# Performance work log

Measured on AMD Instinct MI355X. Metric: run time of the kernel, lower is better.

The kernel has to match this reference:

```python
import jax, jax.numpy as jnp
import numpy as np

S, B, DIN = 3, 4096, 1024
H1, H2, H3, D = 512, 384, 256, 128
K, C = 512, 3            # codebook size, n_codebooks
TEMP = 0.1               # contrastive temperature
EPS = 1e-12


def setup_inputs() -> dict:
    key = jax.random.key(0)
    ks = jax.random.split(key, 16)
    g = lambda k, shp, s=0.05: (jax.random.normal(k, shp, dtype=jnp.float32) * s)
    return {
        'x': jax.random.normal(ks[0], (S, B, DIN), dtype=jnp.float32),
        'enc_w1': g(ks[1], (S, DIN, H1)), 'enc_b1': g(ks[2], (S, H1)),
        'enc_w2': g(ks[3], (S, H1, H2)), 'enc_b2': g(ks[4], (S, H2)),
        'enc_w3': g(ks[5], (S, H2, H3)), 'enc_b3': g(ks[6], (S, H3)),
        'enc_w4': g(ks[7], (S, H3, D)),  'enc_b4': g(ks[8], (S, D)),
        'q_w1': g(ks[9], (D, D)), 'q_b1': g(ks[10], (D,)),
        'q_w2': g(ks[11], (D,)),
        'codebooks': jax.random.normal(ks[12], (C, K, D), dtype=jnp.float32),
    }


def _normalize(v):
    return v / jnp.maximum(jnp.linalg.norm(v, axis=-1, keepdims=True), EPS)


def _forward(x, enc_w1, enc_b1, enc_w2, enc_b2, enc_w3, enc_b3,
             enc_w4, enc_b4, q_w1, q_b1, q_w2, codebooks):
    sg = jax.lax.stop_gradient
    # per-source MLP encoders (stacked over source axis s)
    h = jax.nn.relu(jnp.einsum('sbi,sio->sbo', x, enc_w1) + enc_b1[:, None, :])
    h = jax.nn.relu(jnp.einsum('sbi,sio->sbo', h, enc_w2) + enc_b2[:, None, :])
    h = jax.nn.relu(jnp.einsum('sbi,sio->sbo', h, enc_w3) + enc_b3[:, None, :])
    emb = jnp.einsum('sbi,sio->sbo', h, enc_w4) + enc_b4[:, None, :]  # [S,B,D]

    # attention fusion: Linear->Tanh->Linear(1) per source, softmax over sources
    score = jnp.einsum('sbd,d->sb', jnp.tanh(jnp.einsum('sbd,de->sbe', emb, q_w1) + q_b1), q_w2)
    weight = jax.nn.softmax(score.T, axis=-1)                # [B,S]
    fused = jnp.einsum('bs,sbd->bd', weight, emb)            # [B,D]

    # residual VQ over C codebooks (straight-through, MSE losses)
    res = fused
    q_sum = jnp.zeros_like(fused)
    commit_loss = jnp.float32(0.0)
    for k in range(C):
        e = codebooks[k]                                     # [K,D]
        d2 = (jnp.sum(res * res, axis=1, keepdims=True)
              - 2.0 * res @ e.T + jnp.sum(e * e, axis=1))    # [B,K]
        ids = jnp.argmin(d2, axis=1)
        q = e[ids]                                           # [B,D]
        commit_loss = commit_loss + jnp.mean((sg(q) - res) ** 2)
        q_st = res + sg(q - res)                             # straight-through
        q_sum = q_sum + q_st
        res = res - q_st

    # codebook regularizer: mean pairwise cosine gram of normalized codebooks
    cbn = _normalize(codebooks)
    codebook_loss = jnp.mean(jnp.einsum('mkd,mjd->mkj', cbn, cbn))

    # contrastive losses (projection = identity)
    z1 = _normalize(q_sum)                                   # [B,D]
    contrast = []
    for s in range(S):
        z2 = _normalize(emb[s])
        refl = jnp.exp((z1 @ z1.T) / TEMP)                   # [B,B]
        between = jnp.exp((z1 @ z2.T) / TEMP)
        pos = jnp.diagonal(between)
        denom = refl.sum(1) + between.sum(1) - jnp.diagonal(refl)
        contrast.append(jnp.mean(-jnp.log(pos / denom)))

    return jnp.stack([1.0 * codebook_loss, 0.0 * commit_loss] + contrast)


def reference(x, enc_w1, enc_b1, enc_w2, enc_b2, enc_w3, enc_b3,
              enc_w4, enc_b4, q_w1, q_b1, q_w2, codebooks):
    return _forward(x, enc_w1, enc_b1, enc_w2, enc_b2, enc_w3, enc_b3,
                    enc_w4, enc_b4, q_w1, q_b1, q_w2, codebooks)
```

## Files before the change

kernel.cpp:

```cpp
#include <hip/hip_runtime.h>
#include <hip/hip_bf16.h>

#define S_   3
#define B_   4096
#define DIN_ 1024
#define H1_  512
#define H2_  384
#define H3_  256
#define D_   128
#define K_   512
#define C_   3
#define INV_T 10.0f
#define EPS_  1e-12f
#define EXP10 22026.465794806718f

typedef float f32x4 __attribute__((ext_vector_type(4)));
typedef short bf16x8 __attribute__((ext_vector_type(8)));

__device__ __forceinline__ unsigned short f2bf(float f) {
  unsigned int u = __float_as_uint(f);
  u = (u + 0x7FFF + ((u >> 16) & 1)) >> 16;
  return (unsigned short)u;
}

__device__ __forceinline__ void gl2lds16(const unsigned short* g, unsigned short* l) {
  __builtin_amdgcn_global_load_lds(
      (const __attribute__((address_space(1))) void*)g,
      (__attribute__((address_space(3))) void*)l, 16, 0, 0);
}

__device__ __forceinline__ float waveReduceSum(float v) {
#pragma unroll
  for (int off = 32; off > 0; off >>= 1) v += __shfl_down(v, off, 64);
  return v;
}

__device__ __forceinline__ float waveXorSum(float v) {
#pragma unroll
  for (int off = 32; off > 0; off >>= 1) v += __shfl_xor(v, off, 64);
  return v;
}

__global__ __launch_bounds__(256) void prep_kernel(
    const float* __restrict__ x, unsigned short* __restrict__ xb,
    const float* __restrict__ w1, unsigned short* __restrict__ wt1,
    const float* __restrict__ w2, unsigned short* __restrict__ wt2,
    const float* __restrict__ w3, unsigned short* __restrict__ wt3,
    const float* __restrict__ w4, unsigned short* __restrict__ w4tb,
    const float* __restrict__ cb, float* __restrict__ cbn2,
    float* __restrict__ cbsumP, unsigned short* __restrict__ cbb,
    const float* __restrict__ qw1, unsigned short* __restrict__ qw1tb) {
  __shared__ float tt[32][33];
  __shared__ float invn[64];
  const int t = threadIdx.x;
  int blk = blockIdx.x;
  const int NCVT = (S_ * B_ * DIN_) / 1024;
  if (blk < NCVT) {
    int i = (blk * 256 + t) * 4;
    float4 v = *(const float4*)(x + i);
    xb[i + 0] = f2bf(v.x); xb[i + 1] = f2bf(v.y);
    xb[i + 2] = f2bf(v.z); xb[i + 3] = f2bf(v.w);
    return;
  }
  blk -= NCVT;
  const int NT = 1536 + 576 + 288 + 96;
  if (blk >= NT) {
    int cblk = blk - NT;
    if (cblk < 24) {
      const int m = cblk >> 3;
      const int k0 = (cblk & 7) * 64;
      const int w = t >> 6, lane = t & 63;
      for (int r = w * 16; r < w * 16 + 16; r++) {
        int k = k0 + r;
        float2 v = *(const float2*)(cb + ((size_t)m * K_ + k) * D_ + lane * 2);
        unsigned short* crow = cbb + ((size_t)m * K_ + k) * D_;
        crow[lane * 2 + 0] = f2bf(v.x);
        crow[lane * 2 + 1] = f2bf(v.y);
        float n2 = waveXorSum(v.x * v.x + v.y * v.y);
        if (lane == 0) {
          cbn2[m * K_ + k] = n2;
          invn[r] = 1.0f / fmaxf(sqrtf(n2), EPS_);
        }
      }
      __syncthreads();
      if (t < D_) {
        float acc = 0.0f;
        for (int r = 0; r < 64; r++)
          acc += cb[((size_t)m * K_ + k0 + r) * D_ + t] * invn[r];
        cbsumP[(size_t)cblk * D_ + t] = acc;
      }
      return;
    }
    cblk -= 24;
    const int kx = cblk & 3, ny = cblk >> 2;
    const int k0 = kx * 32, n0 = ny * 32;
    const int tx = t & 31, ty = t >> 5;
#pragma unroll
    for (int i = 0; i < 4; i++)
      tt[ty + 8 * i][tx] = qw1[(size_t)(k0 + ty + 8 * i) * D_ + n0 + tx];
    __syncthreads();
#pragma unroll
    for (int i = 0; i < 4; i++)
      qw1tb[(size_t)(n0 + ty + 8 * i) * D_ + k0 + tx] = f2bf(tt[tx][ty + 8 * i]);
    return;
  }
  const float* W; unsigned short* Wt; int K, N; int plain = 0;
  if (blk < 1536) { W = w1; Wt = wt1; K = DIN_; N = H1_; }
  else {
    blk -= 1536;
    if (blk < 576) { W = w2; Wt = wt2; K = H1_; N = H2_; }
    else {
      blk -= 576;
      if (blk < 288) { W = w3; Wt = wt3; K = H2_; N = H3_; }
      else { blk -= 288; W = w4; Wt = w4tb; K = H3_; N = D_; plain = 1; }
    }
  }
  const int kx_n = K / 32, ny_n = N / 32;
  const int kx = blk % kx_n;
  const int ny = (blk / kx_n) % ny_n;
  const int s  = blk / (kx_n * ny_n);
  const int k0 = kx * 32, n0 = ny * 32;
  const int tx = t & 31, ty = t >> 5;
  const float* Ws = W + (size_t)s * K * N;
  const int nb = N >> 7, kb = K >> 6;
#pragma unroll
  for (int i = 0; i < 4; i++)
    tt[ty + 8 * i][tx] = Ws[(size_t)(k0 + ty + 8 * i) * N + n0 + tx];
  __syncthreads();
  const int k = k0 + tx;
  if (plain) {
#pragma unroll
    for (int i = 0; i < 4; i++) {
      int n = n0 + ty + 8 * i;
      Wt[((size_t)(s * D_ + n)) * H3_ + k] = f2bf(tt[tx][ty + 8 * i]);
    }
  } else {
    const int kt = k >> 6, ksl = (k >> 5) & 1;
#pragma unroll
    for (int i = 0; i < 4; i++) {
      int n = n0 + ty + 8 * i;
      size_t dst = ((size_t)(s * nb + (n >> 7)) * kb + kt) * 8192 +
                   (size_t)ksl * 4096 + (size_t)(n & 127) * 32 + (k & 31);
      Wt[dst] = f2bf(tt[tx][ty + 8 * i]);
    }
  }
}

__global__ __launch_bounds__(256) void gemm_lds_kernel(
    const unsigned short* __restrict__ A, const unsigned short* __restrict__ Wsw,
    const float* __restrict__ bias, void* __restrict__ Y,
    int K, int N, int relu, int out_f32) {
  const int t = threadIdx.x;
  const int lane = t & 63;
  const int w = t >> 6;
  const int ln = lane & 15, q = lane >> 4;
  const int wm = w >> 1, wn = w & 1;
  const int n0 = blockIdx.x * 128;
  const int mblk = blockIdx.y;
  const int s = mblk >> 6;
  const int m0 = mblk * 64;
  const int nb = N >> 7, kb = K >> 6;

  const unsigned short* Ag = A + (size_t)m0 * K;
  const unsigned short* Bt = Wsw + ((size_t)(s * nb + blockIdx.x) * kb) * 8192;
  const float* bs = bias + (size_t)s * N;

  __shared__ unsigned short Asm[2 * 64 * 32];
  __shared__ unsigned short Bsm[2 * 8192];

  const int arow0 = t >> 3, ak8 = t & 7;
  const int aL0 = (ak8 >> 2) * 2048 + arow0 * 32 + (ak8 & 3) * 8;
  const size_t gA0 = (size_t)arow0 * K + ak8 * 8;

  bf16x8 ra0 = *(const bf16x8*)(Ag + gA0);
  bf16x8 ra1 = *(const bf16x8*)(Ag + gA0 + (size_t)32 * K);
#pragma unroll
  for (int p = 0; p < 4; p++)
    gl2lds16(Bt + (size_t)(p * 256 + t) * 8, &Bsm[(size_t)(p * 256 + t) * 8]);

  f32x4 acc[2][4];
#pragma unroll
  for (int i = 0; i < 2; i++)
#pragma unroll
    for (int j = 0; j < 4; j++) acc[i][j] = (f32x4){0.f, 0.f, 0.f, 0.f};

  for (int kt = 0; kt < kb; kt++) {
    *(bf16x8*)&Asm[aL0] = ra0;
    *(bf16x8*)&Asm[aL0 + 1024] = ra1;
    __syncthreads();
    const unsigned short* Bcur = &Bsm[(kt & 1) * 8192];
    if (kt + 1 < kb) {
      const unsigned short* Bn = Bt + (size_t)(kt + 1) * 8192;
      unsigned short* Bd = &Bsm[((kt + 1) & 1) * 8192];
#pragma unroll
      for (int p = 0; p < 4; p++)
        gl2lds16(Bn + (size_t)(p * 256 + t) * 8, Bd + (size_t)(p * 256 + t) * 8);
      const size_t g = gA0 + (size_t)(kt + 1) * 64;
      ra0 = *(const bf16x8*)(Ag + g);
      ra1 = *(const bf16x8*)(Ag + g + (size_t)32 * K);
    }
    bf16x8 af[2][2], bf[4][2];
#pragma unroll
    for (int ti = 0; ti < 2; ti++)
#pragma unroll
      for (int ksl = 0; ksl < 2; ksl++)
        af[ti][ksl] = *(const bf16x8*)&Asm[ksl * 2048 + (wm * 32 + ti * 16 + ln) * 32 + q * 8];
#pragma unroll
    for (int tj = 0; tj < 4; tj++)
#pragma unroll
      for (int ksl = 0; ksl < 2; ksl++)
        bf[tj][ksl] = *(const bf16x8*)&Bcur[ksl * 4096 + (wn * 64 + tj * 16 + ln) * 32 + q * 8];
#pragma unroll
    for (int ksl = 0; ksl < 2; ksl++)
#pragma unroll
      for (int ti = 0; ti < 2; ti++)
#pragma unroll
        for (int tj = 0; tj < 4; tj++)
          acc[ti][tj] = __builtin_amdgcn_mfma_f32_16x16x32_bf16(af[ti][ksl], bf[tj][ksl], acc[ti][tj], 0, 0, 0);
    __syncthreads();
  }

#pragma unroll
  for (int ti = 0; ti < 2; ti++)
#pragma unroll
    for (int tj = 0; tj < 4; tj++) {
      const int cc = n0 + wn * 64 + tj * 16 + ln;
      const float bv = bs[cc];
#pragma unroll
      for (int reg = 0; reg < 4; reg++) {
        const int r = m0 + wm * 32 + ti * 16 + q * 4 + reg;
        float v = acc[ti][tj][reg] + bv;
        if (relu) v = fmaxf(v, 0.0f);
        if (out_f32) ((float*)Y)[(size_t)r * N + cc] = v;
        else ((unsigned short*)Y)[(size_t)r * N + cc] = f2bf(v);
      }
    }
}

__global__ __launch_bounds__(512) void l4vq_kernel(
    const unsigned short* __restrict__ h3b, const unsigned short* __restrict__ w4tb,
    const float* __restrict__ b4, const unsigned short* __restrict__ qw1tb,
    const float* __restrict__ qb1, const float* __restrict__ qw2,
    const float* __restrict__ cb, const unsigned short* __restrict__ cbb,
    const float* __restrict__ cbn2,
    unsigned short* __restrict__ zb, float* __restrict__ pos) {
  const int b0 = blockIdx.x * 16;
  const int t = threadIdx.x;
  const int w = t >> 6, lane = t & 63;
  const int ln = lane & 15, q = lane >> 4;

  __shared__ unsigned short h3s[48][264];
  __shared__ float e[48][D_];
  __shared__ unsigned short ebb[48][136];
  __shared__ float qf[16][D_];
  __shared__ float resv[16][D_];
  __shared__ unsigned short resb[16][136];
  __shared__ float red2[8][48];
  __shared__ float sc[48];
  __shared__ float candd[8][16];
  __shared__ int candk[8][16];
  __shared__ int bestk[16];

  bf16x8 bq[4];
  {
    const unsigned short* qp = qw1tb + (size_t)(w * 16 + ln) * D_;
#pragma unroll
    for (int ks = 0; ks < 4; ks++)
      bq[ks] = *(const bf16x8*)(qp + ks * 32 + q * 8);
  }

#pragma unroll
  for (int p = 0; p < 3; p++) {
    int f = p * 512 + t;
    int r = f >> 5, kf = f & 31;
    int s = r >> 4, bi = r & 15;
    *(bf16x8*)&h3s[r][kf * 8] =
        *(const bf16x8*)(h3b + ((size_t)(s * B_ + b0 + bi)) * H3_ + kf * 8);
  }
  __syncthreads();

  {
    const int col = w * 16 + ln;
#pragma unroll
    for (int s = 0; s < 3; s++) {
      f32x4 oacc = (f32x4){0.f, 0.f, 0.f, 0.f};
      const unsigned short* wp = w4tb + ((size_t)(s * D_ + col)) * H3_;
#pragma unroll
      for (int ks = 0; ks < 8; ks++) {
        bf16x8 bfrag = *(const bf16x8*)(wp + ks * 32 + q * 8);
        bf16x8 afrag = *(const bf16x8*)&h3s[s * 16 + ln][ks * 32 + q * 8];
        oacc = __builtin_amdgcn_mfma_f32_16x16x32_bf16(afrag, bfrag, oacc, 0, 0, 0);
      }
      const float bv = b4[s * D_ + col];
#pragma unroll
      for (int reg = 0; reg < 4; reg++) {
        int r = s * 16 + q * 4 + reg;
        float v = oacc[reg] + bv;
        e[r][col] = v;
        ebb[r][col] = f2bf(v);
      }
    }
  }
  __syncthreads();

  {
    f32x4 sacc[3];
#pragma unroll
    for (int rt = 0; rt < 3; rt++) sacc[rt] = (f32x4){0.f, 0.f, 0.f, 0.f};
#pragma unroll
    for (int ks = 0; ks < 4; ks++) {
#pragma unroll
      for (int rt = 0; rt < 3; rt++) {
        bf16x8 a = *(const bf16x8*)&ebb[rt * 16 + ln][ks * 32 + q * 8];
        sacc[rt] = __builtin_amdgcn_mfma_f32_16x16x32_bf16(a, bq[ks], sacc[rt], 0, 0, 0);
      }
    }
    const int col = w * 16 + ln;
    const float qb = qb1[col], q2v = qw2[col];
#pragma unroll
    for (int rt = 0; rt < 3; rt++)
#pragma unroll
      for (int reg = 0; reg < 4; reg++) {
        float v = tanhf(sacc[rt][reg] + qb) * q2v;
#pragma unroll
        for (int off = 8; off > 0; off >>= 1) v += __shfl_xor(v, off, 16);
        if (ln == 0) red2[w][rt * 16 + q * 4 + reg] = v;
      }
  }
  __syncthreads();
  if (t < 48) {
    float s = 0.f;
#pragma unroll
    for (int ww = 0; ww < 8; ww++) s += red2[ww][t];
    sc[t] = s;
  }
  __syncthreads();

#pragma unroll
  for (int p = 0; p < 4; p++) {
    int idx = p * 512 + t;
    int bi = idx >> 7, dd = idx & 127;
    float s0 = sc[bi], s1 = sc[16 + bi], s2 = sc[32 + bi];
    float mx = fmaxf(s0, fmaxf(s1, s2));
    float e0 = __expf(s0 - mx), e1 = __expf(s1 - mx), e2 = __expf(s2 - mx);
    float inv = 1.0f / (e0 + e1 + e2);
    float fv = (e0 * e[bi][dd] + e1 * e[16 + bi][dd] + e2 * e[32 + bi][dd]) * inv;
    qf[bi][dd] = fv;
    resv[bi][dd] = fv;
    resb[bi][dd] = f2bf(fv);
  }
  __syncthreads();

  for (int c = 0; c < C_; c++) {
    bf16x8 a[4];
#pragma unroll
    for (int ks = 0; ks < 4; ks++)
      a[ks] = *(const bf16x8*)&resb[ln][ks * 32 + q * 8];
    f32x4 acc[4];
#pragma unroll
    for (int tt = 0; tt < 4; tt++) acc[tt] = (f32x4){0.f, 0.f, 0.f, 0.f};
#pragma unroll
    for (int tt = 0; tt < 4; tt++) {
      const int n = w * 64 + tt * 16 + ln;
      const unsigned short* bp = cbb + ((size_t)c * K_ + n) * D_;
#pragma unroll
      for (int ks = 0; ks < 4; ks++) {
        bf16x8 b = *(const bf16x8*)(bp + ks * 32 + q * 8);
        acc[tt] = __builtin_amdgcn_mfma_f32_16x16x32_bf16(a[ks], b, acc[tt], 0, 0, 0);
      }
    }
    float bd[4]; int bk[4];
#pragma unroll
    for (int reg = 0; reg < 4; reg++) { bd[reg] = 3.4e38f; bk[reg] = 0x7fffffff; }
#pragma unroll
    for (int tt = 0; tt < 4; tt++) {
      const int col = w * 64 + tt * 16 + ln;
      const float n2 = cbn2[c * K_ + col];
#pragma unroll
      for (int reg = 0; reg < 4; reg++) {
        float dist = n2 - 2.0f * acc[tt][reg];
        if (dist < bd[reg] || (dist == bd[reg] && col < bk[reg])) { bd[reg] = dist; bk[reg] = col; }
      }
    }
#pragma unroll
    for (int reg = 0; reg < 4; reg++) {
#pragma unroll
      for (int off = 8; off > 0; off >>= 1) {
        float d1 = __shfl_down(bd[reg], off, 16);
        int k1 = __shfl_down(bk[reg], off, 16);
        if (d1 < bd[reg] || (d1 == bd[reg] && k1 < bk[reg])) { bd[reg] = d1; bk[reg] = k1; }
      }
      if (ln == 0) { candd[w][q * 4 + reg] = bd[reg]; candk[w][q * 4 + reg] = bk[reg]; }
    }
    __syncthreads();
    if (w == 0) {
      int row = lane >> 2, g = lane & 3;
      float d0 = candd[2 * g][row]; int k0 = candk[2 * g][row];
      float d1 = candd[2 * g + 1][row]; int k1 = candk[2 * g + 1][row];
      if (d1 < d0 || (d1 == d0 && k1 < k0)) { d0 = d1; k0 = k1; }
#pragma unroll
      for (int off = 2; off > 0; off >>= 1) {
        float dn = __shfl_down(d0, off, 4);
        int kn = __shfl_down(k0, off, 4);
        if (dn < d0 || (dn == d0 && kn < k0)) { d0 = dn; k0 = kn; }
      }
      if (g == 0) bestk[row] = k0;
    }
    __syncthreads();
    {
      int idx = t * 4;
      int r = idx >> 7, dd = idx & 127;
      const float4 qv = *(const float4*)(cb + ((size_t)c * K_ + bestk[r]) * D_ + dd);
      float4 rv = *(float4*)&resv[r][dd];
      rv.x -= qv.x; rv.y -= qv.y; rv.z -= qv.z; rv.w -= qv.w;
      *(float4*)&resv[r][dd] = rv;
      resb[r][dd + 0] = f2bf(rv.x); resb[r][dd + 1] = f2bf(rv.y);
      resb[r][dd + 2] = f2bf(rv.z); resb[r][dd + 3] = f2bf(rv.w);
    }
    __syncthreads();
  }

  {
    int idx = t * 4;
    int r = idx >> 7, dd = idx & 127;
    float4 f = *(float4*)&qf[r][dd];
    float4 rv = *(float4*)&resv[r][dd];
    f.x -= rv.x; f.y -= rv.y; f.z -= rv.z; f.w -= rv.w;
    *(float4*)&qf[r][dd] = f;
  }
  __syncthreads();

#pragma unroll
  for (int rr = 0; rr < 2; rr++) {
    int r = w * 2 + rr;
    float2 v = *(const float2*)&qf[r][lane * 2];
    float n2 = waveXorSum(v.x * v.x + v.y * v.y);
    float inv = 1.0f / fmaxf(sqrtf(n2), EPS_);
    float zx = v.x * inv, zy = v.y * inv;
    zb[(size_t)(b0 + r) * D_ + lane * 2 + 0] = f2bf(zx);
    zb[(size_t)(b0 + r) * D_ + lane * 2 + 1] = f2bf(zy);
    qf[r][lane * 2] = zx; qf[r][lane * 2 + 1] = zy;
  }
  __syncthreads();

#pragma unroll
  for (int rr = 0; rr < 6; rr++) {
    int r = w * 6 + rr;
    int s = r >> 4, bi = r & 15;
    float2 v = *(const float2*)&e[r][lane * 2];
    float n2 = waveXorSum(v.x * v.x + v.y * v.y);
    float inv = 1.0f / fmaxf(sqrtf(n2), EPS_);
    float zx = v.x * inv, zy = v.y * inv;
    size_t gb = (size_t)(1 + s) * B_ + b0 + bi;
    zb[gb * D_ + lane * 2 + 0] = f2bf(zx);
    zb[gb * D_ + lane * 2 + 1] = f2bf(zy);
    float2 a1 = *(const float2*)&qf[bi][lane * 2];
    float dsum = waveXorSum(a1.x * zx + a1.y * zy);
    if (lane == 0) pos[s * B_ + b0 + bi] = dsum;
  }
}

__global__ __launch_bounds__(256) void contrast_mfma_kernel(
    const unsigned short* __restrict__ zb, float* __restrict__ rsP) {
  const int jc = blockIdx.x, ib = blockIdx.y, m = blockIdx.z;
  const int t = threadIdx.x;
  const int w = t >> 6, lane = t & 63;
  const int ln = lane & 15, q = lane >> 4;
  const int i0 = ib * 128 + w * 32;
  const unsigned short* Za = zb;
  const unsigned short* Zm = zb + (size_t)m * B_ * D_;

  __shared__ unsigned short Zsm[64 * 136];

  bf16x8 a[2][4];
#pragma unroll
  for (int si = 0; si < 2; si++)
#pragma unroll
    for (int ks = 0; ks < 4; ks++)
      a[si][ks] = *(const bf16x8*)(Za + (size_t)(i0 + si * 16 + ln) * D_ + ks * 32 + q * 8);

  const unsigned short* tb = Zm + (size_t)(jc * 1024) * D_;
  bf16x8 rz[4];
#pragma unroll
  for (int p = 0; p < 4; p++)
    rz[p] = *(const bf16x8*)(tb + t * 8 + p * 2048);

  float e[2][4] = {};
  for (int jt = 0; jt < 16; jt++) {
#pragma unroll
    for (int p = 0; p < 4; p++) {
      int c = t + p * 256;
      *(bf16x8*)&Zsm[(c >> 4) * 136 + (c & 15) * 8] = rz[p];
    }
    __syncthreads();
    if (jt + 1 < 16) {
      const unsigned short* tn = Zm + (size_t)(jc * 1024 + (jt + 1) * 64) * D_;
#pragma unroll
      for (int p = 0; p < 4; p++)
        rz[p] = *(const bf16x8*)(tn + t * 8 + p * 2048);
    }
    f32x4 acc[2][4];
#pragma unroll
    for (int si = 0; si < 2; si++)
#pragma unroll
      for (int tj = 0; tj < 4; tj++) acc[si][tj] = (f32x4){0.f, 0.f, 0.f, 0.f};
#pragma unroll
    for (int tj = 0; tj < 4; tj++) {
      bf16x8 b[4];
#pragma unroll
      for (int ks = 0; ks < 4; ks++)
        b[ks] = *(const bf16x8*)&Zsm[(tj * 16 + ln) * 136 + ks * 32 + q * 8];
#pragma unroll
      for (int ks = 0; ks < 4; ks++) {
        acc[0][tj] = __builtin_amdgcn_mfma_f32_16x16x32_bf16(a[0][ks], b[ks], acc[0][tj], 0, 0, 0);
        acc[1][tj] = __builtin_amdgcn_mfma_f32_16x16x32_bf16(a[1][ks], b[ks], acc[1][tj], 0, 0, 0);
      }
    }
#pragma unroll
    for (int si = 0; si < 2; si++)
#pragma unroll
      for (int reg = 0; reg < 4; reg++) {
        float s = 0.f;
#pragma unroll
        for (int tj = 0; tj < 4; tj++) s += __expf(acc[si][tj][reg] * INV_T);
        e[si][reg] += s;
      }
    __syncthreads();
  }
#pragma unroll
  for (int si = 0; si < 2; si++)
#pragma unroll
    for (int reg = 0; reg < 4; reg++) {
#pragma unroll
      for (int off = 8; off > 0; off >>= 1)
        e[si][reg] += __shfl_xor(e[si][reg], off, 16);
    }
  if (ln == 0) {
#pragma unroll
    for (int si = 0; si < 2; si++)
#pragma unroll
      for (int reg = 0; reg < 4; reg++)
        rsP[((size_t)m * 4 + jc) * B_ + i0 + si * 16 + q * 4 + reg] = e[si][reg];
  }
}

__global__ __launch_bounds__(256) void final2_kernel(const float* __restrict__ rsP,
                                                     const float* __restrict__ pos,
                                                     const float* __restrict__ cbsumP,
                                                     float* __restrict__ out) {
  const int blk = blockIdx.x;
  const int t = threadIdx.x;
  __shared__ float red[4];
  if (blk == 0) {
    float acc = 0.0f;
    if (t < D_) {
#pragma unroll
      for (int m = 0; m < C_; m++) {
        float v = 0.0f;
#pragma unroll
        for (int b8 = 0; b8 < 8; b8++) v += cbsumP[(size_t)(m * 8 + b8) * D_ + t];
        acc += v * v;
      }
    }
    float v = waveReduceSum(acc);
    if ((t & 63) == 0) red[t >> 6] = v;
    __syncthreads();
    if (t == 0) {
      out[0] = (red[0] + red[1] + red[2] + red[3]) * (1.0f / (3.0f * 512.0f * 512.0f));
      out[1] = 0.0f;
    }
  } else {
    const int s = blk - 1;
    float acc = 0.0f;
    for (int it = 0; it < 16; it++) {
      const int i = it * 256 + t;
      float denom = -EXP10;
#pragma unroll
      for (int jc = 0; jc < 4; jc++) {
        denom += rsP[(size_t)jc * B_ + i];
        denom += rsP[((size_t)(1 + s) * 4 + jc) * B_ + i];
      }
      acc += logf(denom) - pos[s * B_ + i] * INV_T;
    }
    float v = waveReduceSum(acc);
    if ((t & 63) == 0) red[t >> 6] = v;
    __syncthreads();
    if (t == 0)
      out[2 + s] = (red[0] + red[1] + red[2] + red[3]) * (1.0f / 4096.0f);
  }
}

extern "C" void kernel_launch(void* const* d_in, const int* in_sizes, int n_in,
                              void* d_out, int out_size, void* d_ws, size_t ws_size,
                              hipStream_t stream) {
  const float* x    = (const float*)d_in[0];
  const float* w1   = (const float*)d_in[1];
  const float* b1   = (const float*)d_in[2];
  const float* w2   = (const float*)d_in[3];
  const float* b2   = (const float*)d_in[4];
  const float* w3   = (const float*)d_in[5];
  const float* b3   = (const float*)d_in[6];
  const float* w4   = (const float*)d_in[7];
  const float* b4   = (const float*)d_in[8];
  const float* qw1  = (const float*)d_in[9];
  const float* qb1  = (const float*)d_in[10];
  const float* qw2  = (const float*)d_in[11];
  const float* cb   = (const float*)d_in[12];
  float* out = (float*)d_out;
  char* base = (char*)d_ws;

  size_t o = 0;
  auto alloc = [&](size_t bytes) { size_t r = o; o += (bytes + 255) & ~(size_t)255; return r; };
  size_t o_xb   = alloc((size_t)S_ * B_ * DIN_ * 2);
  size_t o_wt1  = alloc((size_t)S_ * H1_ * DIN_ * 2);
  size_t o_wt2  = alloc((size_t)S_ * H2_ * H1_ * 2);
  size_t o_wt3  = alloc((size_t)S_ * H3_ * H2_ * 2);
  size_t o_w4t  = alloc((size_t)S_ * D_ * H3_ * 2);
  size_t o_h1b  = alloc((size_t)S_ * B_ * H1_ * 2);
  size_t o_h2b  = alloc((size_t)S_ * B_ * H2_ * 2);
  size_t o_h3b  = alloc((size_t)S_ * B_ * H3_ * 2);
  size_t o_zb   = alloc((size_t)4 * B_ * D_ * 2);
  size_t o_cbn2 = alloc((size_t)C_ * K_ * 4);
  size_t o_cbb  = alloc((size_t)C_ * K_ * D_ * 2);
  size_t o_rsP  = alloc((size_t)4 * 4 * B_ * 4);
  size_t o_cbsP = alloc((size_t)C_ * 8 * D_ * 4);
  size_t o_pos  = alloc((size_t)S_ * B_ * 4);
  size_t o_q1t  = alloc((size_t)D_ * D_ * 2);
  (void)ws_size; (void)in_sizes; (void)n_in; (void)out_size;

  unsigned short* xb  = (unsigned short*)(base + o_xb);
  unsigned short* wt1 = (unsigned short*)(base + o_wt1);
  unsigned short* wt2 = (unsigned short*)(base + o_wt2);
  unsigned short* wt3 = (unsigned short*)(base + o_wt3);
  unsigned short* w4tb= (unsigned short*)(base + o_w4t);
  unsigned short* h1b = (unsigned short*)(base + o_h1b);
  unsigned short* h2b = (unsigned short*)(base + o_h2b);
  unsigned short* h3b = (unsigned short*)(base + o_h3b);
  unsigned short* zb = (unsigned short*)(base + o_zb);
  float* cbn2  = (float*)(base + o_cbn2);
  unsigned short* cbb = (unsigned short*)(base + o_cbb);
  float* rsP   = (float*)(base + o_rsP);
  float* cbsumP= (float*)(base + o_cbsP);
  float* pos   = (float*)(base + o_pos);
  unsigned short* qw1tb = (unsigned short*)(base + o_q1t);

  const int prep_blocks = (S_ * B_ * DIN_) / 1024 + 1536 + 576 + 288 + 96 + C_ * 8 + 16;
  prep_kernel<<<dim3(prep_blocks), 256, 0, stream>>>(x, xb, w1, wt1, w2, wt2, w3, wt3, w4, w4tb,
                                                     cb, cbn2, cbsumP, cbb, qw1, qw1tb);

  const int Mtot = S_ * B_;
  gemm_lds_kernel<<<dim3(H1_ / 128, Mtot / 64), 256, 0, stream>>>(xb, wt1, b1, h1b, DIN_, H1_, 1, 0);
  gemm_lds_kernel<<<dim3(H2_ / 128, Mtot / 64), 256, 0, stream>>>(h1b, wt2, b2, h2b, H1_, H2_, 1, 0);
  gemm_lds_kernel<<<dim3(H3_ / 128, Mtot / 64), 256, 0, stream>>>(h2b, wt3, b3, h3b, H2_, H3_, 1, 0);

  l4vq_kernel<<<dim3(B_ / 16), 512, 0, stream>>>(h3b, w4tb, b4, qw1tb, qb1, qw2,
                                                 cb, cbb, cbn2, zb, pos);

  contrast_mfma_kernel<<<dim3(4, 32, 4), 256, 0, stream>>>(zb, rsP);

  final2_kernel<<<dim3(4), 256, 0, stream>>>(rsP, pos, cbsumP, out);
}
```

Measured before the change: 240.1 us.

## Process 8 batch rows per l4vq block to double grid size

The fused layer-4/attention/VQ kernel now handles 8 batch rows per block instead of 16, launching twice as many blocks to spread work across more CUs. Each wave now owns one row, so the argmin reduction, residual update and normalization are done per wave without a separate cross-wave pass and barrier. The cost is that the MFMA tiles are half-filled (16-row tiles holding 8 valid rows), and the codebook and weight fragments are reloaded by twice as many blocks.

```diff
diff --git a/kernel.cpp b/kernel.cpp
--- a/kernel.cpp
+++ b/kernel.cpp
@@ -244,22 +244,21 @@
     const float* __restrict__ cb, const unsigned short* __restrict__ cbb,
     const float* __restrict__ cbn2,
     unsigned short* __restrict__ zb, float* __restrict__ pos) {
-  const int b0 = blockIdx.x * 16;
+  const int b0 = blockIdx.x * 8;
   const int t = threadIdx.x;
   const int w = t >> 6, lane = t & 63;
   const int ln = lane & 15, q = lane >> 4;
 
-  __shared__ unsigned short h3s[48][264];
-  __shared__ float e[48][D_];
-  __shared__ unsigned short ebb[48][136];
-  __shared__ float qf[16][D_];
-  __shared__ float resv[16][D_];
+  __shared__ unsigned short h3s[32][264];
+  __shared__ float e[24][D_];
+  __shared__ unsigned short ebb[32][136];
+  __shared__ float qf[8][D_];
+  __shared__ float resv[8][D_];
   __shared__ unsigned short resb[16][136];
-  __shared__ float red2[8][48];
-  __shared__ float sc[48];
+  __shared__ float red2[8][24];
+  __shared__ float sc[24];
   __shared__ float candd[8][16];
   __shared__ int candk[8][16];
-  __shared__ int bestk[16];
 
   bf16x8 bq[4];
   {
@@ -270,12 +269,14 @@
   }
 
 #pragma unroll
-  for (int p = 0; p < 3; p++) {
+  for (int p = 0; p < 2; p++) {
     int f = p * 512 + t;
-    int r = f >> 5, kf = f & 31;
-    int s = r >> 4, bi = r & 15;
-    *(bf16x8*)&h3s[r][kf * 8] =
-        *(const bf16x8*)(h3b + ((size_t)(s * B_ + b0 + bi)) * H3_ + kf * 8);
+    if (f < 768) {
+      int r = f >> 5, kf = f & 31;
+      int s = r >> 3, bi = r & 7;
+      *(bf16x8*)&h3s[r][kf * 8] =
+          *(const bf16x8*)(h3b + ((size_t)(s * B_ + b0 + bi)) * H3_ + kf * 8);
+    }
   }
   __syncthreads();
 
@@ -288,29 +289,31 @@
 #pragma unroll
       for (int ks = 0; ks < 8; ks++) {
         bf16x8 bfrag = *(const bf16x8*)(wp + ks * 32 + q * 8);
-        bf16x8 afrag = *(const bf16x8*)&h3s[s * 16 + ln][ks * 32 + q * 8];
+        bf16x8 afrag = *(const bf16x8*)&h3s[s * 8 + ln][ks * 32 + q * 8];
         oacc = __builtin_amdgcn_mfma_f32_16x16x32_bf16(afrag, bfrag, oacc, 0, 0, 0);
       }
-      const float bv = b4[s * D_ + col];
-#pragma unroll
-      for (int reg = 0; reg < 4; reg++) {
-        int r = s * 16 + q * 4 + reg;
-        float v = oacc[reg] + bv;
-        e[r][col] = v;
-        ebb[r][col] = f2bf(v);
+      if (q < 2) {
+        const float bv = b4[s * D_ + col];
+#pragma unroll
+        for (int reg = 0; reg < 4; reg++) {
+          int rr = q * 4 + reg;
+          float v = oacc[reg] + bv;
+          e[s * 8 + rr][col] = v;
+          ebb[s * 8 + rr][col] = f2bf(v);
+        }
       }
     }
   }
   __syncthreads();
 
   {
-    f32x4 sacc[3];
-#pragma unroll
-    for (int rt = 0; rt < 3; rt++) sacc[rt] = (f32x4){0.f, 0.f, 0.f, 0.f};
+    f32x4 sacc[2];
+#pragma unroll
+    for (int rt = 0; rt < 2; rt++) sacc[rt] = (f32x4){0.f, 0.f, 0.f, 0.f};
 #pragma unroll
     for (int ks = 0; ks < 4; ks++) {
 #pragma unroll
-      for (int rt = 0; rt < 3; rt++) {
+      for (int rt = 0; rt < 2; rt++) {
         bf16x8 a = *(const bf16x8*)&ebb[rt * 16 + ln][ks * 32 + q * 8];
         sacc[rt] = __builtin_amdgcn_mfma_f32_16x16x32_bf16(a, bq[ks], sacc[rt], 0, 0, 0);
       }
@@ -318,17 +321,18 @@
     const int col = w * 16 + ln;
     const float qb = qb1[col], q2v = qw2[col];
 #pragma unroll
-    for (int rt = 0; rt < 3; rt++)
+    for (int rt = 0; rt < 2; rt++)
 #pragma unroll
       for (int reg = 0; reg < 4; reg++) {
+        int rr = rt * 16 + q * 4 + reg;
         float v = tanhf(sacc[rt][reg] + qb) * q2v;
 #pragma unroll
         for (int off = 8; off > 0; off >>= 1) v += __shfl_xor(v, off, 16);
-        if (ln == 0) red2[w][rt * 16 + q * 4 + reg] = v;
+        if (rr < 24 && ln == 0) red2[w][rr] = v;
       }
   }
   __syncthreads();
-  if (t < 48) {
+  if (t < 24) {
     float s = 0.f;
 #pragma unroll
     for (int ww = 0; ww < 8; ww++) s += red2[ww][t];
@@ -336,18 +340,21 @@
   }
   __syncthreads();
 
-#pragma unroll
-  for (int p = 0; p < 4; p++) {
-    int idx = p * 512 + t;
-    int bi = idx >> 7, dd = idx & 127;
-    float s0 = sc[bi], s1 = sc[16 + bi], s2 = sc[32 + bi];
+  {
+    float s0 = sc[w], s1 = sc[8 + w], s2 = sc[16 + w];
     float mx = fmaxf(s0, fmaxf(s1, s2));
     float e0 = __expf(s0 - mx), e1 = __expf(s1 - mx), e2 = __expf(s2 - mx);
     float inv = 1.0f / (e0 + e1 + e2);
-    float fv = (e0 * e[bi][dd] + e1 * e[16 + bi][dd] + e2 * e[32 + bi][dd]) * inv;
-    qf[bi][dd] = fv;
-    resv[bi][dd] = fv;
-    resb[bi][dd] = f2bf(fv);
+    int dd = lane * 2;
+    float2 a0 = *(const float2*)&e[w][dd];
+    float2 a1 = *(const float2*)&e[8 + w][dd];
+    float2 a2 = *(const float2*)&e[16 + w][dd];
+    float fx = (e0 * a0.x + e1 * a1.x + e2 * a2.x) * inv;
+    float fy = (e0 * a0.y + e1 * a1.y + e2 * a2.y) * inv;
+    *(float2*)&qf[w][dd] = make_float2(fx, fy);
+    *(float2*)&resv[w][dd] = make_float2(fx, fy);
+    resb[w][dd + 0] = f2bf(fx);
+    resb[w][dd + 1] = f2bf(fy);
   }
   __syncthreads();
 
@@ -393,68 +400,51 @@
       if (ln == 0) { candd[w][q * 4 + reg] = bd[reg]; candk[w][q * 4 + reg] = bk[reg]; }
     }
     __syncthreads();
-    if (w == 0) {
-      int row = lane >> 2, g = lane & 3;
-      float d0 = candd[2 * g][row]; int k0 = candk[2 * g][row];
-      float d1 = candd[2 * g + 1][row]; int k1 = candk[2 * g + 1][row];
-      if (d1 < d0 || (d1 == d0 && k1 < k0)) { d0 = d1; k0 = k1; }
-#pragma unroll
-      for (int off = 2; off > 0; off >>= 1) {
-        float dn = __shfl_down(d0, off, 4);
-        int kn = __shfl_down(k0, off, 4);
-        if (dn < d0 || (dn == d0 && kn < k0)) { d0 = dn; k0 = kn; }
-      }
-      if (g == 0) bestk[row] = k0;
-    }
-    __syncthreads();
+    float d0 = candd[0][w]; int k0c = candk[0][w];
+#pragma unroll
+    for (int ww = 1; ww < 8; ww++) {
+      float d1 = candd[ww][w]; int k1 = candk[ww][w];
+      if (d1 < d0 || (d1 == d0 && k1 < k0c)) { d0 = d1; k0c = k1; }
+    }
     {
-      int idx = t * 4;
-      int r = idx >> 7, dd = idx & 127;
-      const float4 qv = *(const float4*)(cb + ((size_t)c * K_ + bestk[r]) * D_ + dd);
-      float4 rv = *(float4*)&resv[r][dd];
-      rv.x -= qv.x; rv.y -= qv.y; rv.z -= qv.z; rv.w -= qv.w;
-      *(float4*)&resv[r][dd] = rv;
-      resb[r][dd + 0] = f2bf(rv.x); resb[r][dd + 1] = f2bf(rv.y);
-      resb[r][dd + 2] = f2bf(rv.z); resb[r][dd + 3] = f2bf(rv.w);
-    }
-    __syncthreads();
+      int dd = lane * 2;
+      float2 qv = *(const float2*)(cb + ((size_t)c * K_ + k0c) * D_ + dd);
+      float2 rv = *(float2*)&resv[w][dd];
+      rv.x -= qv.x; rv.y -= qv.y;
+      *(float2*)&resv[w][dd] = rv;
+      resb[w][dd + 0] = f2bf(rv.x);
+      resb[w][dd + 1] = f2bf(rv.y);
+    }
+    if (c < C_ - 1) __syncthreads();
   }
 
   {
-    int idx = t * 4;
-    int r = idx >> 7, dd = idx & 127;
-    float4 f = *(float4*)&qf[r][dd];
-    float4 rv = *(float4*)&resv[r][dd];
-    f.x -= rv.x; f.y -= rv.y; f.z -= rv.z; f.w -= rv.w;
-    *(float4*)&qf[r][dd] = f;
+    int dd = lane * 2;
+    float2 f = *(float2*)&qf[w][dd];
+    float2 rv = *(float2*)&resv[w][dd];
+    float zx0 = f.x - rv.x, zy0 = f.y - rv.y;
+    float n2 = waveXorSum(zx0 * zx0 + zy0 * zy0);
+    float inv = 1.0f / fmaxf(sqrtf(n2), EPS_);
+    float zx = zx0 * inv, zy = zy0 * inv;
+    zb[(size_t)(b0 + w) * D_ + dd + 0] = f2bf(zx);
+    zb[(size_t)(b0 + w) * D_ + dd + 1] = f2bf(zy);
+    qf[w][dd] = zx; qf[w][dd + 1] = zy;
   }
   __syncthreads();
 
 #pragma unroll
-  for (int rr = 0; rr < 2; rr++) {
-    int r = w * 2 + rr;
-    float2 v = *(const float2*)&qf[r][lane * 2];
-    float n2 = waveXorSum(v.x * v.x + v.y * v.y);
-    float inv = 1.0f / fmaxf(sqrtf(n2), EPS_);
-    float zx = v.x * inv, zy = v.y * inv;
-    zb[(size_t)(b0 + r) * D_ + lane * 2 + 0] = f2bf(zx);
-    zb[(size_t)(b0 + r) * D_ + lane * 2 + 1] = f2bf(zy);
-    qf[r][lane * 2] = zx; qf[r][lane * 2 + 1] = zy;
-  }
-  __syncthreads();
-
-#pragma unroll
-  for (int rr = 0; rr < 6; rr++) {
-    int r = w * 6 + rr;
-    int s = r >> 4, bi = r & 15;
-    float2 v = *(const float2*)&e[r][lane * 2];
+  for (int rr = 0; rr < 3; rr++) {
+    int r = w * 3 + rr;
+    int s = r >> 3, bi = r & 7;
+    int dd = lane * 2;
+    float2 v = *(const float2*)&e[r][dd];
     float n2 = waveXorSum(v.x * v.x + v.y * v.y);
     float inv = 1.0f / fmaxf(sqrtf(n2), EPS_);
     float zx = v.x * inv, zy = v.y * inv;
     size_t gb = (size_t)(1 + s) * B_ + b0 + bi;
-    zb[gb * D_ + lane * 2 + 0] = f2bf(zx);
-    zb[gb * D_ + lane * 2 + 1] = f2bf(zy);
-    float2 a1 = *(const float2*)&qf[bi][lane * 2];
+    zb[gb * D_ + dd + 0] = f2bf(zx);
+    zb[gb * D_ + dd + 1] = f2bf(zy);
+    float2 a1 = *(const float2*)&qf[bi][dd];
     float dsum = waveXorSum(a1.x * zx + a1.y * zy);
     if (lane == 0) pos[s * B_ + b0 + bi] = dsum;
   }
@@ -653,8 +643,8 @@
   gemm_lds_kernel<<<dim3(H2_ / 128, Mtot / 64), 256, 0, stream>>>(h1b, wt2, b2, h2b, H1_, H2_, 1, 0);
   gemm_lds_kernel<<<dim3(H3_ / 128, Mtot / 64), 256, 0, stream>>>(h2b, wt3, b3, h3b, H2_, H3_, 1, 0);
 
-  l4vq_kernel<<<dim3(B_ / 16), 512, 0, stream>>>(h3b, w4tb, b4, qw1tb, qb1, qw2,
-                                                 cb, cbb, cbn2, zb, pos);
+  l4vq_kernel<<<dim3(B_ / 8), 512, 0, stream>>>(h3b, w4tb, b4, qw1tb, qb1, qw2,
+                                                cb, cbb, cbn2, zb, pos);
 
   contrast_mfma_kernel<<<dim3(4, 32, 4), 256, 0, stream>>>(zb, rsP);
 
```

Result: slower. 245.2 us (+2.1%).
